# Kernel tuning notes

Measured on AMD Instinct MI355X. Metric: run time of the kernel, lower is better.

Reference implementation:

```python
import jax, jax.numpy as jnp
import numpy as np
from jax import lax

# NSA constants (must match init_kwargs)
STRIDE = 16     # compression_stride
LC = 32         # compression_block
LB = 64         # selection_block
KSEL = 8        # selected_block_count
WIN = 512       # sliding_window
POOL_K = LB // STRIDE + 1   # 5
POOL_S = LB // STRIDE       # 4


def masked_softmax(scores, mask):
    s = jnp.where(mask, scores, -jnp.inf)
    m = jnp.max(s, axis=-1, keepdims=True)
    m = jnp.where(jnp.isfinite(m), m, 0.0)
    p = jnp.where(mask, jnp.exp(s - m), 0.0)
    return p / jnp.maximum(jnp.sum(p, axis=-1, keepdims=True), 1e-20)


def setup_inputs() -> dict:
    key = jax.random.key(0)
    ks = jax.random.split(key, 6)
    S, Hq, Hkv, D = 2048, 16, 2, 64
    q = jax.random.normal(ks[0], (S, Hq, D), jnp.float32)
    k = jax.random.normal(ks[1], (S, Hkv, D), jnp.float32)
    v = jax.random.normal(ks[2], (S, Hkv, D), jnp.float32)
    wk = jax.random.normal(ks[3], (D, D, LC), jnp.float32) * 0.05  # conv1d compressor (OIH)
    wv = jax.random.normal(ks[4], (D, D, LC), jnp.float32) * 0.05
    wg = jax.random.normal(ks[5], (3, D), jnp.float32) * 0.05      # gating Linear weight
    cu_seqlens = jnp.array([0, S], dtype=jnp.int32)
    return {"q": q, "k": k, "v": v, "wk": wk, "wv": wv, "wg": wg, "cu_seqlens": cu_seqlens}


def nsa_forward(q, k, v, wk, wv, wg, cu_seqlens):
    B = cu_seqlens.shape[0] - 1  # static (=1)
    S, Hq, D = q.shape
    Hkv = k.shape[1]
    g = Hq // Hkv
    scale = D ** -0.5
    q = q.reshape(B, S, Hq, D)
    Kt = jnp.transpose(k.reshape(B, S, Hkv, D), (0, 2, 1, 3))  # [B,Hkv,S,D]
    Vt = jnp.transpose(v.reshape(B, S, Hkv, D), (0, 2, 1, 3))
    qg = jnp.transpose(q.reshape(B, S, Hkv, g, D), (0, 2, 3, 1, 4))  # [B,Hkv,g,S,D]
    t_idx = jnp.arange(S)

    # gating scores (Linear weight only, no bias used in source)
    gate = jnp.einsum('bshd,ed->bshe', q, wg)  # [B,S,Hq,3]

    # --- branch 1: compressed-KV attention (conv1d pooling of K/V) ---
    kc = Kt.reshape(B * Hkv, S, D).transpose(0, 2, 1)  # [BH, D, S]
    vc = Vt.reshape(B * Hkv, S, D).transpose(0, 2, 1)
    dn = ('NCH', 'OIH', 'NCH')
    ck = lax.conv_general_dilated(kc, wk, (STRIDE,), 'VALID', dimension_numbers=dn)
    cv = lax.conv_general_dilated(vc, wv, (STRIDE,), 'VALID', dimension_numbers=dn)
    Sc = ck.shape[-1]  # (S-LC)//STRIDE + 1
    ckt = jnp.transpose(ck.reshape(B, Hkv, D, Sc), (0, 1, 3, 2))  # [B,Hkv,Sc,D]
    cvt = jnp.transpose(cv.reshape(B, Hkv, D, Sc), (0, 1, 3, 2))
    sc_c = jnp.einsum('bhgsd,bhcd->bhgsc', qg, ckt) * scale
    j = jnp.arange(Sc)
    mask_c = (j[None, :] * STRIDE + LC) <= (t_idx[:, None] + 1)  # [S,Sc]
    p_c = masked_softmax(sc_c, mask_c)
    cmp_o = jnp.einsum('bhgsc,bhcd->bhgsd', p_c, cvt)

    # --- branch 2: top-k block selection attention ---
    p_kv = p_c.sum(axis=2)  # sum over GQA group heads -> [B,Hkv,S,Sc]
    n_out = (Sc - POOL_K) // POOL_S + 1
    pooled = sum(p_kv[..., t:t + n_out * POOL_S:POOL_S] for t in range(POOL_K)) / POOL_K
    n_blocks = S // LB
    pooled = jnp.pad(pooled, ((0, 0), (0, 0), (0, 0), (0, n_blocks - n_out)),
                     constant_values=-1.0)  # [B,Hkv,S,n_blocks]
    blk_q = t_idx // LB
    block_ids = jnp.arange(n_blocks)
    sel_scores = jnp.where(block_ids[None, :] == blk_q[:, None], jnp.inf, pooled)  # force current block
    _, idx = lax.top_k(sel_scores, KSEL)  # [B,Hkv,S,KSEL]
    pos = (idx[..., None] * LB + jnp.arange(LB)).reshape(B, Hkv, S, KSEL * LB)
    Kg = jnp.take_along_axis(Kt[:, :, None], pos[..., None], axis=3)  # [B,Hkv,S,J,D]
    Vg = jnp.take_along_axis(Vt[:, :, None], pos[..., None], axis=3)
    sc_s = jnp.einsum('bhgsd,bhsjd->bhgsj', qg, Kg) * scale
    mask_s = pos[:, :, None, :, :] <= t_idx[None, None, None, :, None]
    p_s = masked_softmax(sc_s, mask_s)
    sel_o = jnp.einsum('bhgsj,bhsjd->bhgsd', p_s, Vg)

    sc_w = jnp.einsum('bhgsd,bhtd->bhgst', qg, Kt) * scale
    mask_w = (t_idx[None, :] <= t_idx[:, None]) & (t_idx[None, :] >= t_idx[:, None] - (WIN - 1))
    p_w = masked_softmax(sc_w, mask_w)
    swa_o = jnp.einsum('bhgst,bhtd->bhgsd', p_w, Vt)

    # --- fuse via gates: o = g0*sel + g1*swa + g2*cmp ---
    def to_bshd(x):
        return jnp.transpose(x, (0, 3, 1, 2, 4)).reshape(B, S, Hq, D)
    o = (gate[..., 0:1] * to_bshd(sel_o)
         + gate[..., 1:2] * to_bshd(swa_o)
         + gate[..., 2:3] * to_bshd(cmp_o))
    return o.reshape(B * S, Hq, D)


def reference(q, k, v, wk, wv, wg, cu_seqlens):
    return nsa_forward(q, k, v, wk, wv, wg, cu_seqlens)
```

## Files before the change

### kernel.cpp

```cpp
#include <hip/hip_runtime.h>
#include <hip/hip_bf16.h>
#include <math.h>

#define S_LEN  2048
#define HQ     16
#define HKV    2
#define GQ     8
#define DH     64
#define LCC    32
#define CSTRIDE 16
#define SC     127
#define LB     64
#define KSEL   8
#define WIN    512
#define NB     32
#define NOUT   31
#define QTS    8
#define SCALE  0.125f

typedef __attribute__((ext_vector_type(8))) short bf16x8;
typedef __attribute__((ext_vector_type(4))) float f32x4;
typedef unsigned short u16;
typedef unsigned int   u32;

__device__ __forceinline__ u16 f2bf(float f) {
  u32 u = __float_as_uint(f);
  return (u16)((u + 0x7FFFu + ((u >> 16) & 1u)) >> 16);
}

__device__ __forceinline__ void gl_lds16(const void* g, void* lds) {
  __builtin_amdgcn_global_load_lds(
      (const __attribute__((address_space(1))) void*)g,
      (__attribute__((address_space(3))) void*)lds, 16, 0, 0);
}

__global__ __launch_bounds__(256) void nsa_conv_kernel(
    const float* __restrict__ k, const float* __restrict__ v,
    const float* __restrict__ wk, const float* __restrict__ wv,
    float* __restrict__ ck, float* __restrict__ cv) {
  int c = blockIdx.x % SC;
  int h = blockIdx.x / SC;
  __shared__ float kin[LCC * DH];
  __shared__ float vin[LCC * DH];
  __shared__ float cred[128];
  int tid = threadIdx.x;
  for (int f = tid; f < LCC * DH / 4; f += 256) {
    int tt = f >> 4, i4 = f & 15;
    int row = c * CSTRIDE + tt;
    ((float4*)kin)[f] = ((const float4*)(k + ((size_t)row * HKV + h) * DH))[i4];
    ((float4*)vin)[f] = ((const float4*)(v + ((size_t)row * HKV + h) * DH))[i4];
  }
  __syncthreads();
  int o  = tid & 63;
  int kv = (tid >> 6) & 1;
  int uh = tid >> 7;
  const float* w  = (kv ? wv : wk) + (size_t)o * (DH * LCC) + uh * 16;
  const float* in = (kv ? vin : kin) + uh * 16 * DH;
  float acc = 0.f;
  for (int i = 0; i < DH; ++i) {
    #pragma unroll
    for (int u = 0; u < 16; ++u)
      acc = fmaf(in[u * DH + i], w[i * LCC + u], acc);
  }
  if (uh == 1) cred[tid & 127] = acc;
  __syncthreads();
  if (uh == 0) {
    acc += cred[tid & 127];
    float* dst = (kv ? cv : ck);
    dst[((size_t)h * SC + c) * DH + o] = acc;
  }
}

__global__ __launch_bounds__(256) void nsa_prep_kernel(
    const float* __restrict__ q, const float* __restrict__ k,
    const float* __restrict__ v, const float* __restrict__ wg,
    u16* __restrict__ kb, u16* __restrict__ vt, float* __restrict__ gates) {
  int id = blockIdx.x * 256 + threadIdx.x;
  {
    int h = id >> 14, s = (id >> 3) & 2047, d8 = (id & 7) << 3;
    const float4* gp = (const float4*)(k + ((size_t)s * HKV + h) * DH + d8);
    float4 a = gp[0], b = gp[1];
    union { uint4 qv; u16 u[8]; } P;
    P.u[0]=f2bf(a.x); P.u[1]=f2bf(a.y); P.u[2]=f2bf(a.z); P.u[3]=f2bf(a.w);
    P.u[4]=f2bf(b.x); P.u[5]=f2bf(b.y); P.u[6]=f2bf(b.z); P.u[7]=f2bf(b.w);
    *(uint4*)(kb + ((size_t)h * S_LEN + s) * 64 + (d8 ^ ((s & 7) << 3))) = P.qv;
  }
  {
    int h = id >> 14, d = (id >> 8) & 63, s8 = (id & 255) << 3;
    union { uint4 qv; u16 u[8]; } P;
    #pragma unroll
    for (int j = 0; j < 8; ++j)
      P.u[j] = f2bf(v[(size_t)(s8 + j) * (HKV * DH) + h * DH + d]);
    int dst = (s8 & ~63) | ((s8 & 63) ^ ((d & 7) << 3));
    *(uint4*)(vt + ((size_t)h * 64 + d) * S_LEN + dst) = P.qv;
  }
  {
    int s = id >> 4, hq = id & 15;
    const float4* qp = (const float4*)(q + ((size_t)s * HQ + hq) * DH);
    const float4* w0 = (const float4*)(wg);
    const float4* w1 = (const float4*)(wg + DH);
    const float4* w2 = (const float4*)(wg + 2 * DH);
    float g0 = 0.f, g1 = 0.f, g2 = 0.f;
    #pragma unroll
    for (int i = 0; i < 16; ++i) {
      float4 a = qp[i];
      float4 b0 = w0[i], b1 = w1[i], b2 = w2[i];
      g0 += a.x*b0.x + a.y*b0.y + a.z*b0.z + a.w*b0.w;
      g1 += a.x*b1.x + a.y*b1.y + a.z*b1.z + a.w*b1.w;
      g2 += a.x*b2.x + a.y*b2.y + a.z*b2.z + a.w*b2.w;
    }
    float* gp = gates + ((size_t)s * HQ + hq) * 3;
    gp[0] = g0; gp[1] = g1; gp[2] = g2;
  }
}

__global__ __launch_bounds__(256) void nsa_cmp_kernel(
    const float* __restrict__ q, const float* __restrict__ ck,
    const float* __restrict__ cv, const float* __restrict__ gates,
    float* __restrict__ out, int* __restrict__ sel) {
  int h  = blockIdx.x >> 9;
  int s0 = (blockIdx.x & 511) << 2;
  int tid = threadIdx.x;
  int w = tid >> 6, l = tid & 63;
  __shared__ float t4s[SC * DH];
  __shared__ float pbuf[4][GQ][136];
  __shared__ float pkvb[4][128];
  float4* t4 = (float4*)t4s;

  int s  = s0 + w;
  int hq = l >> 3, cg = l & 7;

  {
    const float4* ck4 = (const float4*)(ck + (size_t)h * SC * DH);
    for (int f = tid; f < SC * 16; f += 256) {
      int c = f >> 4, i = f & 15;
      t4[(c << 4) | (i ^ (c & 7))] = ck4[f];
    }
  }
  float4 q4[16];
  {
    const float4* qp = (const float4*)(q + ((size_t)s * HQ + h * GQ + hq) * DH);
    #pragma unroll
    for (int i = 0; i < 16; ++i) q4[i] = qp[i];
  }
  __syncthreads();

  int nc = (s >= LCC - 1) ? ((s - (LCC - 1)) >> 4) + 1 : 0;

  float p[16];
  float m = -INFINITY;
  #pragma unroll
  for (int t = 0; t < 16; ++t) {
    int c = cg + (t << 3);
    float d = 0.f;
    #pragma unroll
    for (int i = 0; i < 16; ++i) {
      float4 kk = t4[(c << 4) | (i ^ cg)];
      d = fmaf(kk.x, q4[i].x, d); d = fmaf(kk.y, q4[i].y, d);
      d = fmaf(kk.z, q4[i].z, d); d = fmaf(kk.w, q4[i].w, d);
    }
    float x = (c < nc) ? d * SCALE : -INFINITY;
    p[t] = x;
    m = fmaxf(m, x);
  }
  m = fmaxf(m, __shfl_xor(m, 1));
  m = fmaxf(m, __shfl_xor(m, 2));
  m = fmaxf(m, __shfl_xor(m, 4));
  m = fmaxf(m, -1e30f);
  float ssum = 0.f;
  #pragma unroll
  for (int t = 0; t < 16; ++t) { p[t] = expf(p[t] - m); ssum += p[t]; }
  ssum += __shfl_xor(ssum, 1);
  ssum += __shfl_xor(ssum, 2);
  ssum += __shfl_xor(ssum, 4);
  float inv = 1.f / fmaxf(ssum, 1e-20f);
  #pragma unroll
  for (int t = 0; t < 16; ++t) {
    p[t] *= inv;
    pbuf[w][hq][cg + (t << 3)] = p[t];
  }
  #pragma unroll
  for (int t = 0; t < 16; ++t) {
    float v0 = p[t];
    v0 += __shfl_xor(v0, 8);
    v0 += __shfl_xor(v0, 16);
    v0 += __shfl_xor(v0, 32);
    p[t] = v0;
  }
  if (hq == 0) {
    #pragma unroll
    for (int t = 0; t < 16; ++t) pkvb[w][cg + (t << 3)] = p[t];
  }
  if (l < 32) {
    float pv;
    if (l < NOUT) {
      float tt = 0.f;
      #pragma unroll
      for (int u = 0; u < 5; ++u) tt += pkvb[w][l * 4 + u];
      pv = tt * 0.2f;
    } else pv = -1.0f;
    if (l == (s >> 6)) pv = INFINITY;
    int* dst = sel + ((size_t)h * S_LEN + s) * KSEL;
    #pragma unroll
    for (int kk = 0; kk < KSEL; ++kk) {
      float v0 = pv; int i0 = l;
      #pragma unroll
      for (int off = 16; off; off >>= 1) {
        float v1 = __shfl_xor(v0, off, 32);
        int   i1 = __shfl_xor(i0, off, 32);
        if (v1 > v0 || (v1 == v0 && i1 < i0)) { v0 = v1; i0 = i1; }
      }
      if (l == 0) dst[kk] = i0;
      if (l == i0) pv = -INFINITY;
    }
  }
  __syncthreads();
  {
    const float4* cv4 = (const float4*)(cv + (size_t)h * SC * DH);
    for (int f = tid; f < SC * 16; f += 256) t4[f] = cv4[f];
  }
  __syncthreads();
  {
    int d4 = l & 15, hg2 = l >> 4;
    float4 a0 = {0.f,0.f,0.f,0.f}, a1 = {0.f,0.f,0.f,0.f};
    #pragma unroll 2
    for (int c = 0; c < nc; ++c) {
      float4 vv = t4[(c << 4) | d4];
      float p0 = pbuf[w][hg2][c];
      float p1 = pbuf[w][hg2 + 4][c];
      a0.x = fmaf(p0, vv.x, a0.x); a0.y = fmaf(p0, vv.y, a0.y);
      a0.z = fmaf(p0, vv.z, a0.z); a0.w = fmaf(p0, vv.w, a0.w);
      a1.x = fmaf(p1, vv.x, a1.x); a1.y = fmaf(p1, vv.y, a1.y);
      a1.z = fmaf(p1, vv.z, a1.z); a1.w = fmaf(p1, vv.w, a1.w);
    }
    float g0 = gates[((size_t)s * HQ + h * GQ + hg2) * 3 + 2];
    float g1 = gates[((size_t)s * HQ + h * GQ + hg2 + 4) * 3 + 2];
    float4 o0, o1;
    o0.x = g0*a0.x; o0.y = g0*a0.y; o0.z = g0*a0.z; o0.w = g0*a0.w;
    o1.x = g1*a1.x; o1.y = g1*a1.y; o1.z = g1*a1.z; o1.w = g1*a1.w;
    ((float4*)(out + ((size_t)s * HQ + h * GQ + hg2) * DH))[d4] = o0;
    ((float4*)(out + ((size_t)s * HQ + h * GQ + hg2 + 4) * DH))[d4] = o1;
  }
}

__device__ __forceinline__ void stage_chunk(const u16* kbh, const u16* vth,
                                            int cb, int w, int l,
                                            short* kT, short* vT) {
  #pragma unroll
  for (int r = 0; r < 2; ++r) {
    int seg = w * 2 + r;
    gl_lds16((const char*)kbh + (size_t)cb * 128 + seg * 1024 + l * 16,
             (char*)kT + seg * 1024);
    int drow = seg * 8 + (l >> 3);
    gl_lds16((const char*)vth + (size_t)drow * (S_LEN * 2) + cb * 2 + (l & 7) * 16,
             (char*)vT + seg * 1024);
  }
}

__device__ __forceinline__ void compute_chunk(
    const short* kT, const short* vT, short* pTw,
    int cb, int lo_l, bool selb, int l, int s_lane,
    const bf16x8 (&qf)[2], f32x4 (&o)[4], float& mrun, float& lsum) {
  int col = l & 15;
  int lg8 = (l >> 4) << 3;
  int kq  = (l >> 4) << 2;
  int xr  = (l & 7) << 3;

  f32x4 st[4];
  #pragma unroll
  for (int mt = 0; mt < 4; ++mt) st[mt] = (f32x4){0.f, 0.f, 0.f, 0.f};
  __builtin_amdgcn_s_setprio(1);
  #pragma unroll
  for (int ks = 0; ks < 2; ++ks) {
    int co = (ks * 32 + lg8) ^ xr;
    #pragma unroll
    for (int mt = 0; mt < 4; ++mt) {
      bf16x8 kf = *(const bf16x8*)(&kT[((mt * 16 + col) << 6) | co]);
      st[mt] = __builtin_amdgcn_mfma_f32_16x16x32_bf16(kf, qf[ks], st[mt], 0, 0, 0);
    }
  }
  __builtin_amdgcn_s_setprio(0);

  float mc = -INFINITY;
  #pragma unroll
  for (int mt = 0; mt < 4; ++mt) {
    #pragma unroll
    for (int r = 0; r < 4; ++r) {
      int key = cb + mt * 16 + kq + r;
      bool vis = selb && (key >= lo_l) && (key <= s_lane);
      float x = vis ? st[mt][r] * SCALE : -INFINITY;
      st[mt][r] = x;
      mc = fmaxf(mc, x);
    }
  }
  mc = fmaxf(mc, __shfl_xor(mc, 16));
  mc = fmaxf(mc, __shfl_xor(mc, 32));
  float mn = fmaxf(fmaxf(mrun, mc), -1e30f);
  float fr = __expf(mrun - mn);
  float ps = 0.f;
  #pragma unroll
  for (int mt = 0; mt < 4; ++mt) {
    #pragma unroll
    for (int r = 0; r < 4; ++r) {
      float p = __expf(st[mt][r] - mn);
      st[mt][r] = p; ps += p;
    }
  }
  ps += __shfl_xor(ps, 16);
  ps += __shfl_xor(ps, 32);
  lsum = lsum * fr + ps;
  mrun = mn;
  #pragma unroll
  for (int mt = 0; mt < 4; ++mt) o[mt] *= fr;

  int pc = col << 6;
  #pragma unroll
  for (int mt = 0; mt < 4; ++mt) {
    #pragma unroll
    for (int pr = 0; pr < 2; ++pr) {
      int key = mt * 16 + kq + pr * 2;
      u32 pk = (u32)f2bf(st[mt][pr * 2]) | ((u32)f2bf(st[mt][pr * 2 + 1]) << 16);
      *(u32*)(&pTw[pc | (key ^ xr)]) = pk;
    }
  }

  __builtin_amdgcn_s_setprio(1);
  #pragma unroll
  for (int ks = 0; ks < 2; ++ks) {
    int co = (ks * 32 + lg8) ^ xr;
    bf16x8 pf = *(const bf16x8*)(&pTw[pc | co]);
    #pragma unroll
    for (int mt = 0; mt < 4; ++mt) {
      bf16x8 vf = *(const bf16x8*)(&vT[((mt * 16 + col) << 6) | co]);
      o[mt] = __builtin_amdgcn_mfma_f32_16x16x32_bf16(vf, pf, o[mt], 0, 0, 0);
    }
  }
  __builtin_amdgcn_s_setprio(0);
}

__global__ __launch_bounds__(256) void nsa_selswa_kernel(
    const float* __restrict__ q, const u16* __restrict__ kb,
    const u16* __restrict__ vt, const float* __restrict__ gates,
    const int* __restrict__ sel, float* __restrict__ out) {
  int bid = blockIdx.x;
  int h  = bid >> 8;
  int s0 = (bid & 255) * QTS;
  int tid = threadIdx.x;
  int w = tid >> 6, l = tid & 63;
  __shared__ __align__(16) short kTb[2][64 * 64];
  __shared__ __align__(16) short vTb[2][64 * 64];
  __shared__ __align__(16) short pT[4][16 * 64];
  __shared__ int selsh[64];

  if (tid < 64)
    selsh[tid] = sel[((size_t)h * S_LEN + s0 + (tid >> 3)) * KSEL + (tid & 7)];

  int col = l & 15, qq = col & 7, gh2 = col >> 3;
  int s_lane = s0 + qq;
  size_t qrow = (size_t)s_lane * HQ + h * 8 + w * 2 + gh2;

  bf16x8 qf[2];
  #pragma unroll
  for (int ks = 0; ks < 2; ++ks) {
    const float4* gp = (const float4*)(q + qrow * DH + ks * 32 + ((l >> 4) << 3));
    float4 a = gp[0], b = gp[1];
    union { bf16x8 v; u16 u[8]; } P;
    P.u[0]=f2bf(a.x); P.u[1]=f2bf(a.y); P.u[2]=f2bf(a.z); P.u[3]=f2bf(a.w);
    P.u[4]=f2bf(b.x); P.u[5]=f2bf(b.y); P.u[6]=f2bf(b.z); P.u[7]=f2bf(b.w);
    qf[ks] = P.v;
  }
  float gsel = gates[qrow * 3 + 0];
  float gswa = gates[qrow * 3 + 1];
  __syncthreads();

  u32 qmask = 0;
  #pragma unroll
  for (int j = 0; j < 8; ++j) qmask |= 1u << selsh[qq * 8 + j];
  u32 un = qmask;
  un |= (u32)__shfl_xor((int)un, 1);
  un |= (u32)__shfl_xor((int)un, 2);
  un |= (u32)__shfl_xor((int)un, 4);

  const u16* kbh = kb + (size_t)h * S_LEN * 64;
  const u16* vth = vt + (size_t)h * 64 * S_LEN;
  short* pTw = pT[w];

  f32x4 o[4];
  f32x4 res[4];
  float mrun, lsum;

  #pragma unroll
  for (int mt = 0; mt < 4; ++mt) o[mt] = (f32x4){0.f, 0.f, 0.f, 0.f};
  mrun = -INFINITY; lsum = 0.f;
  {
    u32 rem = un;
    int cb = __builtin_ctz(rem) << 6;
    int par = 0;
    stage_chunk(kbh, vth, cb, w, l, kTb[0], vTb[0]);
    __syncthreads();
    while (1) {
      u32 rem2 = rem & (rem - 1);
      int cbn = rem2 ? (__builtin_ctz(rem2) << 6) : -1;
      if (cbn >= 0) stage_chunk(kbh, vth, cbn, w, l, kTb[par ^ 1], vTb[par ^ 1]);
      compute_chunk(kTb[par], vTb[par], pTw, cb, 0, (qmask >> (cb >> 6)) & 1,
                    l, s_lane, qf, o, mrun, lsum);
      __syncthreads();
      if (cbn < 0) break;
      rem = rem2; cb = cbn; par ^= 1;
    }
  }
  {
    float gv = gsel / fmaxf(lsum, 1e-20f);
    #pragma unroll
    for (int mt = 0; mt < 4; ++mt) res[mt] = o[mt] * gv;
  }

  #pragma unroll
  for (int mt = 0; mt < 4; ++mt) o[mt] = (f32x4){0.f, 0.f, 0.f, 0.f};
  mrun = -INFINITY; lsum = 0.f;
  {
    int t0 = s0 - (WIN - 1); if (t0 < 0) t0 = 0;
    int lo_l = s_lane - (WIN - 1);
    int cbend = s0 + QTS - 1;
    int cb = t0 & ~63;
    int par = 0;
    stage_chunk(kbh, vth, cb, w, l, kTb[0], vTb[0]);
    __syncthreads();
    while (1) {
      int cbn = (cb + 64 <= cbend) ? cb + 64 : -1;
      if (cbn >= 0) stage_chunk(kbh, vth, cbn, w, l, kTb[par ^ 1], vTb[par ^ 1]);
      compute_chunk(kTb[par], vTb[par], pTw, cb, lo_l, true,
                    l, s_lane, qf, o, mrun, lsum);
      __syncthreads();
      if (cbn < 0) break;
      cb = cbn; par ^= 1;
    }
  }
  {
    float gv = gswa / fmaxf(lsum, 1e-20f);
    #pragma unroll
    for (int mt = 0; mt < 4; ++mt) res[mt] += o[mt] * gv;
  }

  int kq = (l >> 4) << 2;
  #pragma unroll
  for (int mt = 0; mt < 4; ++mt) {
    float4* op = (float4*)(out + qrow * DH + mt * 16 + kq);
    float4 pv = *op;
    pv.x += res[mt][0]; pv.y += res[mt][1];
    pv.z += res[mt][2]; pv.w += res[mt][3];
    *op = pv;
  }
}

extern "C" void kernel_launch(void* const* d_in, const int* in_sizes, int n_in,
                              void* d_out, int out_size, void* d_ws, size_t ws_size,
                              hipStream_t stream) {
  const float* q  = (const float*)d_in[0];
  const float* k  = (const float*)d_in[1];
  const float* v  = (const float*)d_in[2];
  const float* wk = (const float*)d_in[3];
  const float* wv = (const float*)d_in[4];
  const float* wg = (const float*)d_in[5];
  float* out = (float*)d_out;

  float* ck    = (float*)d_ws;
  float* cv    = ck + (size_t)HKV * SC * DH;
  float* gates = cv + (size_t)HKV * SC * DH;
  int*   sel   = (int*)(gates + (size_t)S_LEN * HQ * 3);
  u16*   kb    = (u16*)(sel + (size_t)HKV * S_LEN * KSEL);
  u16*   vt    = kb + (size_t)HKV * S_LEN * DH;

  nsa_conv_kernel<<<HKV * SC, 256, 0, stream>>>(k, v, wk, wv, ck, cv);
  nsa_prep_kernel<<<128, 256, 0, stream>>>(q, k, v, wg, kb, vt, gates);
  nsa_cmp_kernel<<<HKV * (S_LEN / 4), 256, 0, stream>>>(q, ck, cv, gates, out, sel);
  nsa_selswa_kernel<<<HKV * (S_LEN / QTS), 256, 0, stream>>>(q, kb, vt, gates, sel, out);
}
```

Measured before the change: 207.9 us.

## Split selection and sliding-window passes into separate blocks with specialized masking

The fused selection+SWA kernel is split so each branch runs in its own block (doubling the grid). The selection output goes to a workspace buffer, and a small merge kernel adds it into out. If the workspace is too small, two sequential launches are used instead. The change also adds a masked/unmasked template so interior chunks skip per-key masking, folds the scale into q, skips online-softmax rescaling when the max grows by at most 8, clips selected blocks to the causal range, and uses packed bf16 conversion. These aim to raise occupancy and parallelism and to cut VALU work, at the cost of an extra launch, extra global traffic for the merge, and recomputing q loads and staging per pass.

```diff
diff --git a/kernel.cpp b/kernel.cpp
--- a/kernel.cpp
+++ b/kernel.cpp
@@ -257,9 +257,10 @@
   }
 }
 
+template <bool MASKED>
 __device__ __forceinline__ void compute_chunk(
     const short* kT, const short* vT, short* pTw,
-    int cb, int lo_l, bool selb, int l, int s_lane,
+    int cb, int lo_l, u32 span, float selbias, int l,
     const bf16x8 (&qf)[2], f32x4 (&o)[4], float& mrun, float& lsum) {
   int col = l & 15;
   int lg8 = (l >> 4) << 3;
@@ -286,40 +287,49 @@
   for (int mt = 0; mt < 4; ++mt) {
     #pragma unroll
     for (int r = 0; r < 4; ++r) {
-      int key = cb + mt * 16 + kq + r;
-      bool vis = selb && (key >= lo_l) && (key <= s_lane);
-      float x = vis ? st[mt][r] * SCALE : -INFINITY;
+      float x = st[mt][r] + selbias;
+      if (MASKED) {
+        int key = cb + mt * 16 + kq + r;
+        bool vis = (u32)(key - lo_l) <= span;
+        x = vis ? x : -INFINITY;
+      }
       st[mt][r] = x;
       mc = fmaxf(mc, x);
     }
   }
   mc = fmaxf(mc, __shfl_xor(mc, 16));
   mc = fmaxf(mc, __shfl_xor(mc, 32));
-  float mn = fmaxf(fmaxf(mrun, mc), -1e30f);
-  float fr = __expf(mrun - mn);
+
+  if (!__all(mc <= mrun + 8.f)) {
+    float mn = fmaxf(fmaxf(mrun, mc), -1e30f);
+    float fr = __expf(mrun - mn);
+    #pragma unroll
+    for (int mt = 0; mt < 4; ++mt) o[mt] *= fr;
+    lsum *= fr;
+    mrun = mn;
+  }
   float ps = 0.f;
   #pragma unroll
   for (int mt = 0; mt < 4; ++mt) {
     #pragma unroll
     for (int r = 0; r < 4; ++r) {
-      float p = __expf(st[mt][r] - mn);
+      float p = __expf(st[mt][r] - mrun);
       st[mt][r] = p; ps += p;
     }
   }
   ps += __shfl_xor(ps, 16);
   ps += __shfl_xor(ps, 32);
-  lsum = lsum * fr + ps;
-  mrun = mn;
-  #pragma unroll
-  for (int mt = 0; mt < 4; ++mt) o[mt] *= fr;
+  lsum += ps;
 
   int pc = col << 6;
   #pragma unroll
   for (int mt = 0; mt < 4; ++mt) {
     #pragma unroll
     for (int pr = 0; pr < 2; ++pr) {
+      u32 pk;
+      asm("v_cvt_pk_bf16_f32 %0, %1, %2"
+          : "=v"(pk) : "v"(st[mt][pr * 2]), "v"(st[mt][pr * 2 + 1]));
       int key = mt * 16 + kq + pr * 2;
-      u32 pk = (u32)f2bf(st[mt][pr * 2]) | ((u32)f2bf(st[mt][pr * 2 + 1]) << 16);
       *(u32*)(&pTw[pc | (key ^ xr)]) = pk;
     }
   }
@@ -341,16 +351,21 @@
 __global__ __launch_bounds__(256) void nsa_selswa_kernel(
     const float* __restrict__ q, const u16* __restrict__ kb,
     const u16* __restrict__ vt, const float* __restrict__ gates,
-    const int* __restrict__ sel, float* __restrict__ out) {
+    const int* __restrict__ sel, float* __restrict__ out,
+    float* __restrict__ osel, int mode) {
   int bid = blockIdx.x;
-  int h  = bid >> 8;
-  int s0 = (bid & 255) * QTS;
+  int pass, rest;
+  if (mode == 2) { pass = bid >= HKV * 256; rest = bid & (HKV * 256 - 1); }
+  else           { pass = mode; rest = bid; }
+  int h  = rest >> 8;
+  int s0 = (rest & 255) * QTS;
+  int b0 = s0 >> 6;
   int tid = threadIdx.x;
   int w = tid >> 6, l = tid & 63;
   __shared__ __align__(16) short kTb[2][64 * 64];
   __shared__ __align__(16) short vTb[2][64 * 64];
   __shared__ __align__(16) short pT[4][16 * 64];
-  __shared__ int selsh[64];
+  int* selsh = (int*)&pT[0][0];
 
   if (tid < 64)
     selsh[tid] = sel[((size_t)h * S_LEN + s0 + (tid >> 3)) * KSEL + (tid & 7)];
@@ -365,34 +380,32 @@
     const float4* gp = (const float4*)(q + qrow * DH + ks * 32 + ((l >> 4) << 3));
     float4 a = gp[0], b = gp[1];
     union { bf16x8 v; u16 u[8]; } P;
-    P.u[0]=f2bf(a.x); P.u[1]=f2bf(a.y); P.u[2]=f2bf(a.z); P.u[3]=f2bf(a.w);
-    P.u[4]=f2bf(b.x); P.u[5]=f2bf(b.y); P.u[6]=f2bf(b.z); P.u[7]=f2bf(b.w);
+    P.u[0]=f2bf(a.x*SCALE); P.u[1]=f2bf(a.y*SCALE); P.u[2]=f2bf(a.z*SCALE); P.u[3]=f2bf(a.w*SCALE);
+    P.u[4]=f2bf(b.x*SCALE); P.u[5]=f2bf(b.y*SCALE); P.u[6]=f2bf(b.z*SCALE); P.u[7]=f2bf(b.w*SCALE);
     qf[ks] = P.v;
   }
-  float gsel = gates[qrow * 3 + 0];
-  float gswa = gates[qrow * 3 + 1];
+  float gate = gates[qrow * 3 + (pass ? 1 : 0)];
   __syncthreads();
 
   u32 qmask = 0;
   #pragma unroll
   for (int j = 0; j < 8; ++j) qmask |= 1u << selsh[qq * 8 + j];
-  u32 un = qmask;
-  un |= (u32)__shfl_xor((int)un, 1);
-  un |= (u32)__shfl_xor((int)un, 2);
-  un |= (u32)__shfl_xor((int)un, 4);
 
   const u16* kbh = kb + (size_t)h * S_LEN * 64;
   const u16* vth = vt + (size_t)h * 64 * S_LEN;
   short* pTw = pT[w];
 
   f32x4 o[4];
-  f32x4 res[4];
-  float mrun, lsum;
-
   #pragma unroll
   for (int mt = 0; mt < 4; ++mt) o[mt] = (f32x4){0.f, 0.f, 0.f, 0.f};
-  mrun = -INFINITY; lsum = 0.f;
-  {
+  float mrun = -INFINITY, lsum = 0.f;
+
+  if (pass == 0) {
+    u32 un = qmask;
+    un |= (u32)__shfl_xor((int)un, 1);
+    un |= (u32)__shfl_xor((int)un, 2);
+    un |= (u32)__shfl_xor((int)un, 4);
+    un &= (2u << b0) - 1;
     u32 rem = un;
     int cb = __builtin_ctz(rem) << 6;
     int par = 0;
@@ -402,55 +415,69 @@
       u32 rem2 = rem & (rem - 1);
       int cbn = rem2 ? (__builtin_ctz(rem2) << 6) : -1;
       if (cbn >= 0) stage_chunk(kbh, vth, cbn, w, l, kTb[par ^ 1], vTb[par ^ 1]);
-      compute_chunk(kTb[par], vTb[par], pTw, cb, 0, (qmask >> (cb >> 6)) & 1,
-                    l, s_lane, qf, o, mrun, lsum);
+      float selbias = ((qmask >> (cb >> 6)) & 1) ? 0.f : -INFINITY;
+      if (cb == b0 * 64)
+        compute_chunk<true>(kTb[par], vTb[par], pTw, cb, 0, (u32)s_lane,
+                            selbias, l, qf, o, mrun, lsum);
+      else
+        compute_chunk<false>(kTb[par], vTb[par], pTw, cb, 0, 0,
+                             selbias, l, qf, o, mrun, lsum);
       __syncthreads();
       if (cbn < 0) break;
       rem = rem2; cb = cbn; par ^= 1;
     }
-  }
-  {
-    float gv = gsel / fmaxf(lsum, 1e-20f);
-    #pragma unroll
-    for (int mt = 0; mt < 4; ++mt) res[mt] = o[mt] * gv;
-  }
-
-  #pragma unroll
-  for (int mt = 0; mt < 4; ++mt) o[mt] = (f32x4){0.f, 0.f, 0.f, 0.f};
-  mrun = -INFINITY; lsum = 0.f;
-  {
+  } else {
     int t0 = s0 - (WIN - 1); if (t0 < 0) t0 = 0;
     int lo_l = s_lane - (WIN - 1);
-    int cbend = s0 + QTS - 1;
     int cb = t0 & ~63;
+    int cbt = b0 * 64;
     int par = 0;
     stage_chunk(kbh, vth, cb, w, l, kTb[0], vTb[0]);
     __syncthreads();
     while (1) {
-      int cbn = (cb + 64 <= cbend) ? cb + 64 : -1;
+      int cbn = (cb < cbt) ? cb + 64 : -1;
       if (cbn >= 0) stage_chunk(kbh, vth, cbn, w, l, kTb[par ^ 1], vTb[par ^ 1]);
-      compute_chunk(kTb[par], vTb[par], pTw, cb, lo_l, true,
-                    l, s_lane, qf, o, mrun, lsum);
+      if ((cb + 504 < s0) || (cb == cbt))
+        compute_chunk<true>(kTb[par], vTb[par], pTw, cb, lo_l, (u32)(WIN - 1),
+                            0.f, l, qf, o, mrun, lsum);
+      else
+        compute_chunk<false>(kTb[par], vTb[par], pTw, cb, 0, 0,
+                             0.f, l, qf, o, mrun, lsum);
       __syncthreads();
       if (cbn < 0) break;
       cb = cbn; par ^= 1;
     }
   }
-  {
-    float gv = gswa / fmaxf(lsum, 1e-20f);
-    #pragma unroll
-    for (int mt = 0; mt < 4; ++mt) res[mt] += o[mt] * gv;
-  }
-
+
+  float gv = gate / fmaxf(lsum, 1e-20f);
   int kq = (l >> 4) << 2;
-  #pragma unroll
-  for (int mt = 0; mt < 4; ++mt) {
-    float4* op = (float4*)(out + qrow * DH + mt * 16 + kq);
-    float4 pv = *op;
-    pv.x += res[mt][0]; pv.y += res[mt][1];
-    pv.z += res[mt][2]; pv.w += res[mt][3];
-    *op = pv;
-  }
+  if (mode == 2 && pass == 0) {
+    #pragma unroll
+    for (int mt = 0; mt < 4; ++mt) {
+      float4 pv;
+      pv.x = gv * o[mt][0]; pv.y = gv * o[mt][1];
+      pv.z = gv * o[mt][2]; pv.w = gv * o[mt][3];
+      *(float4*)(osel + qrow * DH + mt * 16 + kq) = pv;
+    }
+  } else {
+    #pragma unroll
+    for (int mt = 0; mt < 4; ++mt) {
+      float4* op = (float4*)(out + qrow * DH + mt * 16 + kq);
+      float4 pv = *op;
+      pv.x = fmaf(gv, o[mt][0], pv.x); pv.y = fmaf(gv, o[mt][1], pv.y);
+      pv.z = fmaf(gv, o[mt][2], pv.z); pv.w = fmaf(gv, o[mt][3], pv.w);
+      *op = pv;
+    }
+  }
+}
+
+__global__ __launch_bounds__(256) void nsa_merge_kernel(
+    const float* __restrict__ osel, float* __restrict__ out) {
+  int i = blockIdx.x * 256 + threadIdx.x;
+  float4 a = ((const float4*)osel)[i];
+  float4 b = ((float4*)out)[i];
+  b.x += a.x; b.y += a.y; b.z += a.z; b.w += a.w;
+  ((float4*)out)[i] = b;
 }
 
 extern "C" void kernel_launch(void* const* d_in, const int* in_sizes, int n_in,
@@ -470,9 +497,17 @@
   int*   sel   = (int*)(gates + (size_t)S_LEN * HQ * 3);
   u16*   kb    = (u16*)(sel + (size_t)HKV * S_LEN * KSEL);
   u16*   vt    = kb + (size_t)HKV * S_LEN * DH;
+  float* osel  = (float*)(vt + (size_t)HKV * DH * S_LEN);
+  size_t need  = (size_t)((char*)(osel + (size_t)S_LEN * HQ * DH) - (char*)d_ws);
 
   nsa_conv_kernel<<<HKV * SC, 256, 0, stream>>>(k, v, wk, wv, ck, cv);
   nsa_prep_kernel<<<128, 256, 0, stream>>>(q, k, v, wg, kb, vt, gates);
   nsa_cmp_kernel<<<HKV * (S_LEN / 4), 256, 0, stream>>>(q, ck, cv, gates, out, sel);
-  nsa_selswa_kernel<<<HKV * (S_LEN / QTS), 256, 0, stream>>>(q, kb, vt, gates, sel, out);
-}
+  if (ws_size >= need) {
+    nsa_selswa_kernel<<<2 * HKV * 256, 256, 0, stream>>>(q, kb, vt, gates, sel, out, osel, 2);
+    nsa_merge_kernel<<<(S_LEN * HQ * DH / 4) / 256, 256, 0, stream>>>(osel, out);
+  } else {
+    nsa_selswa_kernel<<<HKV * 256, 256, 0, stream>>>(q, kb, vt, gates, sel, out, osel, 0);
+    nsa_selswa_kernel<<<HKV * 256, 256, 0, stream>>>(q, kb, vt, gates, sel, out, osel, 1);
+  }
+}
```

Result: faster. 190.6 us (-8.3%).
